# Kernel tuning notes

Measured on AMD Instinct MI355X. Metric: run time of the kernel, lower is better.

Reference implementation:

```python
import jax, jax.numpy as jnp
import numpy as np

B, I, O, H = 16384, 32, 64, 64  # batch, inp_dim, out_dim (towers), hidden width


def setup_inputs() -> dict:
    key = jax.random.key(0)
    ks = jax.random.split(key, 5)
    s0 = 1.0 / np.sqrt(I)
    sh = 1.0 / np.sqrt(H)
    return {
        "x": jax.random.normal(ks[0], (B, I), dtype=jnp.float32),
        "W0": jax.random.normal(ks[1], (O, I, H), dtype=jnp.float32) * s0,
        "b0": jnp.zeros((O, H), dtype=jnp.float32),
        "W1": jax.random.normal(ks[2], (O, H, H), dtype=jnp.float32) * sh,
        "b1": jnp.zeros((O, H), dtype=jnp.float32),
        "W2": jax.random.normal(ks[3], (O, H, H), dtype=jnp.float32) * sh,
        "b2": jnp.zeros((O, H), dtype=jnp.float32),
        "W3": jax.random.normal(ks[4], (O, H), dtype=jnp.float32) * sh,
        "b3": jnp.zeros((O,), dtype=jnp.float32),
    }


def reference(x, W0, b0, W1, b1, W2, b2, W3, b3):
    # O independent towers: Dense(H,relu) x3 then Dense(1); concat along axis=1.
    # Expressed as batched einsums over the tower axis 'o' (same math as the loop).
    h = jax.nn.relu(jnp.einsum('bi,oih->boh', x, W0) + b0)   # [B,O,H]
    h = jax.nn.relu(jnp.einsum('boh,ohk->bok', h, W1) + b1)  # [B,O,H]
    h = jax.nn.relu(jnp.einsum('boh,ohk->bok', h, W2) + b2)  # [B,O,H]
    out = jnp.einsum('boh,oh->bo', h, W3) + b3               # [B,O]
    return out
```

## Files before the change

kernel.cpp:

```cpp
#include <hip/hip_runtime.h>


typedef float  f32x4 __attribute__((ext_vector_type(4)));
typedef _Float16 h8  __attribute__((ext_vector_type(8)));
typedef unsigned int uint4v __attribute__((ext_vector_type(4)));

static constexpr int Bsz  = 16384;
static constexpr int Idim = 32;
static constexpr int Odim = 64;
static constexpr int BPT  = 8;
static constexpr int ROWTILES = (Bsz / 64) / BPT;

static constexpr int IMG = 21504;

#define GLD16(gp, lp) __builtin_amdgcn_global_load_lds( \
    (const __attribute__((address_space(1))) void*)(gp), \
    (__attribute__((address_space(3))) void*)(lp), 16, 0, 0)

__device__ __forceinline__ unsigned short f2h(float f) {
    _Float16 h = (_Float16)f;
    return __builtin_bit_cast(unsigned short, h);
}

__device__ __forceinline__ unsigned cvt_relu_pk(float lo, float hi) {
    unsigned v = __builtin_bit_cast(unsigned, __builtin_amdgcn_cvt_pkrtz(lo, hi));
    unsigned r;
    asm("v_pk_max_f16 %0, %1, 0" : "=v"(r) : "v"(v));
    return r;
}

__device__ __forceinline__ unsigned cvt_pk2(float lo, float hi) {
    return __builtin_bit_cast(unsigned, __builtin_amdgcn_cvt_pkrtz(lo, hi));
}

__device__ __forceinline__ int pi_slot(int in) {
    return 32 * (in >> 5) + 8 * ((in >> 2) & 3) + 4 * ((in >> 4) & 1) + (in & 3);
}

__global__ __launch_bounds__(256) void prep_kernel(
    const float* __restrict__ W0, const float* __restrict__ b0,
    const float* __restrict__ W1, const float* __restrict__ b1,
    const float* __restrict__ W2, const float* __restrict__ b2,
    const float* __restrict__ W3, char* __restrict__ ws)
{
    const int o = blockIdx.x >> 2, q = blockIdx.x & 3, tid = threadIdx.x;
    char* img = ws + o * IMG;
    unsigned short* Wt0 = (unsigned short*)img;
    unsigned short* Wt1 = (unsigned short*)(img + 4096);
    unsigned short* Wt2 = (unsigned short*)(img + 12288);
    unsigned short* w3s = (unsigned short*)(img + 20480);
    float*          bsf = (float*)(img + 20608);

    {
        int f = q * 256 + tid;
        f32x4 v1 = *(const f32x4*)&W1[o * 4096 + f * 4];
        f32x4 v2 = *(const f32x4*)&W2[o * 4096 + f * 4];
        int in = (f * 4) >> 6;
        int h0 = (f * 4) & 63;
        int S  = pi_slot(in);
#pragma unroll
        for (int j = 0; j < 4; ++j) {
            int h = h0 + j;
            int cw = S ^ ((((h >> 2) ^ h) & 7) << 3);
            Wt1[h * 64 + cw] = f2h(v1[j]);
            Wt2[h * 64 + cw] = f2h(v2[j]);
        }
    }
    if (q < 2) {
        int f = q * 256 + tid;
        f32x4 v = *(const f32x4*)&W0[o * 2048 + f * 4];
        int i  = (f * 4) >> 6;
        int h0 = (f * 4) & 63;
#pragma unroll
        for (int j = 0; j < 4; ++j) {
            int h = h0 + j;
            Wt0[h * 32 + (i ^ ((((h >> 2) ^ h) & 3) << 3))] = f2h(v[j]);
        }
    }
    if (q == 3 && tid < 64) {
        w3s[pi_slot(tid)] = f2h(W3[o * 64 + tid]);
        bsf[tid]       = b0[o * 64 + tid];
        bsf[64 + tid]  = b1[o * 64 + tid];
        bsf[128 + tid] = b2[o * 64 + tid];
    }
}

__global__ __launch_bounds__(256, 2) void towers_kernel(
    const float* __restrict__ x, const char* __restrict__ ws,
    const float* __restrict__ b3, float* __restrict__ out)
{
    __shared__ __align__(16) char SH[IMG];

    const int tid  = threadIdx.x;
    const int o    = blockIdx.x / BPT;
    const int slot = blockIdx.x % BPT;
    const int l = tid & 63, w = tid >> 6;
    const int c = l & 15,  g = l >> 4;

    const float* xbase = x + (slot * ROWTILES * 64 + w * 16 + c) * Idim + g * 8;
    f32x4 nxa0 = *(const f32x4*)(xbase);
    f32x4 nxb0 = *(const f32x4*)(xbase + 4);
    f32x4 nxa1 = *(const f32x4*)(xbase + 2048);
    f32x4 nxb1 = *(const f32x4*)(xbase + 2052);

    {
        const char* img = ws + o * IMG;
#pragma unroll
        for (int ch = 0; ch < 6; ++ch) {
            int k = ch * 4 + w;
            if (k < 21)
                GLD16(img + k * 1024 + l * 16, SH + k * 1024);
        }
    }
    __syncthreads();

    const unsigned short* Wt0 = (const unsigned short*)SH;
    const unsigned short* Wt1 = (const unsigned short*)(SH + 4096);
    const unsigned short* w3s = (const unsigned short*)(SH + 20480);
    const float*          bsf = (const float*)(SH + 20608);

    h8 wf0[4], wf1f[4][2];
#pragma unroll
    for (int n = 0; n < 4; ++n) {
        int h = n * 16 + c;
        wf0[n] = *(const h8*)&Wt0[h * 32 + ((g * 8) ^ ((((h >> 2) ^ h) & 3) << 3))];
        int key = ((h >> 2) ^ h) & 7;
#pragma unroll
        for (int s = 0; s < 2; ++s)
            wf1f[n][s] = *(const h8*)&Wt1[h * 64 + ((s * 32 + g * 8) ^ (key << 3))];
    }
    h8 w3a[2];
    w3a[0] = *(const h8*)&w3s[g * 8];
    w3a[1] = *(const h8*)&w3s[32 + g * 8];

    int off2[4][2];
#pragma unroll
    for (int n = 0; n < 4; ++n) {
        int h = n * 16 + c;
        int key = ((h >> 2) ^ h) & 7;
#pragma unroll
        for (int s = 0; s < 2; ++s)
            off2[n][s] = 12288 + 2 * (h * 64 + ((s * 32 + g * 8) ^ (key << 3)));
    }

    f32x4 b0f[4], b1f[4], b2f[4];
#pragma unroll
    for (int n = 0; n < 4; ++n) {
        b0f[n] = *(const f32x4*)&bsf[      n * 16 + g * 4];
        b1f[n] = *(const f32x4*)&bsf[ 64 + n * 16 + g * 4];
        b2f[n] = *(const f32x4*)&bsf[128 + n * 16 + g * 4];
    }
    f32x4 c3 = {0.f, 0.f, 0.f, 0.f};
    if (g == 0) c3[0] = b3[o];

    float* obase = out + (slot * ROWTILES * 64 + w * 16 + c) * Odim + o;

    for (int tt = 0; tt < ROWTILES; tt += 2) {
        f32x4 xa0 = nxa0, xb0 = nxb0, xa1 = nxa1, xb1 = nxb1;
        if (tt + 2 < ROWTILES) {
            const float* np = xbase + (tt + 2) * 2048;
            nxa0 = *(const f32x4*)(np);
            nxb0 = *(const f32x4*)(np + 4);
            nxa1 = *(const f32x4*)(np + 2048);
            nxb1 = *(const f32x4*)(np + 2052);
        }

        uint4v xd0, xd1;
        xd0.x = cvt_pk2(xa0[0], xa0[1]); xd0.y = cvt_pk2(xa0[2], xa0[3]);
        xd0.z = cvt_pk2(xb0[0], xb0[1]); xd0.w = cvt_pk2(xb0[2], xb0[3]);
        xd1.x = cvt_pk2(xa1[0], xa1[1]); xd1.y = cvt_pk2(xa1[2], xa1[3]);
        xd1.z = cvt_pk2(xb1[0], xb1[1]); xd1.w = cvt_pk2(xb1[2], xb1[3]);
        h8 a0_0 = __builtin_bit_cast(h8, xd0);
        h8 a0_1 = __builtin_bit_cast(h8, xd1);

        f32x4 acc0[4], acc1[4];
#pragma unroll
        for (int n = 0; n < 4; ++n) {
            acc0[n] = __builtin_amdgcn_mfma_f32_16x16x32_f16(wf0[n], a0_0, b0f[n], 0, 0, 0);
            acc1[n] = __builtin_amdgcn_mfma_f32_16x16x32_f16(wf0[n], a0_1, b0f[n], 0, 0, 0);
        }

        unsigned p0[4][2], p1[4][2];
#pragma unroll
        for (int n = 0; n < 4; ++n) {
            p0[n][0] = cvt_relu_pk(acc0[n][0], acc0[n][1]);
            p0[n][1] = cvt_relu_pk(acc0[n][2], acc0[n][3]);
            p1[n][0] = cvt_relu_pk(acc1[n][0], acc1[n][1]);
            p1[n][1] = cvt_relu_pk(acc1[n][2], acc1[n][3]);
        }
        h8 Blo0 = __builtin_bit_cast(h8, uint4v{p0[0][0], p0[0][1], p0[1][0], p0[1][1]});
        h8 Bhi0 = __builtin_bit_cast(h8, uint4v{p0[2][0], p0[2][1], p0[3][0], p0[3][1]});
        h8 Blo1 = __builtin_bit_cast(h8, uint4v{p1[0][0], p1[0][1], p1[1][0], p1[1][1]});
        h8 Bhi1 = __builtin_bit_cast(h8, uint4v{p1[2][0], p1[2][1], p1[3][0], p1[3][1]});

#pragma unroll
        for (int n = 0; n < 4; ++n) {
            acc0[n] = __builtin_amdgcn_mfma_f32_16x16x32_f16(wf1f[n][0], Blo0, b1f[n], 0, 0, 0);
            acc1[n] = __builtin_amdgcn_mfma_f32_16x16x32_f16(wf1f[n][0], Blo1, b1f[n], 0, 0, 0);
            acc0[n] = __builtin_amdgcn_mfma_f32_16x16x32_f16(wf1f[n][1], Bhi0, acc0[n], 0, 0, 0);
            acc1[n] = __builtin_amdgcn_mfma_f32_16x16x32_f16(wf1f[n][1], Bhi1, acc1[n], 0, 0, 0);
        }
#pragma unroll
        for (int n = 0; n < 4; ++n) {
            p0[n][0] = cvt_relu_pk(acc0[n][0], acc0[n][1]);
            p0[n][1] = cvt_relu_pk(acc0[n][2], acc0[n][3]);
            p1[n][0] = cvt_relu_pk(acc1[n][0], acc1[n][1]);
            p1[n][1] = cvt_relu_pk(acc1[n][2], acc1[n][3]);
        }
        Blo0 = __builtin_bit_cast(h8, uint4v{p0[0][0], p0[0][1], p0[1][0], p0[1][1]});
        Bhi0 = __builtin_bit_cast(h8, uint4v{p0[2][0], p0[2][1], p0[3][0], p0[3][1]});
        Blo1 = __builtin_bit_cast(h8, uint4v{p1[0][0], p1[0][1], p1[1][0], p1[1][1]});
        Bhi1 = __builtin_bit_cast(h8, uint4v{p1[2][0], p1[2][1], p1[3][0], p1[3][1]});

        {
            const char* base = (const char*)SH;
            h8 w2[4];
#pragma unroll
            for (int n = 0; n < 4; ++n) {
                int a = off2[n][0];
                asm("" : "+v"(a));
                w2[n] = *(const h8*)(base + a);
            }
#pragma unroll
            for (int n = 0; n < 4; ++n) {
                acc0[n] = __builtin_amdgcn_mfma_f32_16x16x32_f16(w2[n], Blo0, b2f[n], 0, 0, 0);
                acc1[n] = __builtin_amdgcn_mfma_f32_16x16x32_f16(w2[n], Blo1, b2f[n], 0, 0, 0);
            }
#pragma unroll
            for (int n = 0; n < 4; ++n) {
                int a = off2[n][1];
                asm("" : "+v"(a));
                w2[n] = *(const h8*)(base + a);
            }
#pragma unroll
            for (int n = 0; n < 4; ++n) {
                acc0[n] = __builtin_amdgcn_mfma_f32_16x16x32_f16(w2[n], Bhi0, acc0[n], 0, 0, 0);
                acc1[n] = __builtin_amdgcn_mfma_f32_16x16x32_f16(w2[n], Bhi1, acc1[n], 0, 0, 0);
            }
        }
#pragma unroll
        for (int n = 0; n < 4; ++n) {
            p0[n][0] = cvt_relu_pk(acc0[n][0], acc0[n][1]);
            p0[n][1] = cvt_relu_pk(acc0[n][2], acc0[n][3]);
            p1[n][0] = cvt_relu_pk(acc1[n][0], acc1[n][1]);
            p1[n][1] = cvt_relu_pk(acc1[n][2], acc1[n][3]);
        }
        Blo0 = __builtin_bit_cast(h8, uint4v{p0[0][0], p0[0][1], p0[1][0], p0[1][1]});
        Bhi0 = __builtin_bit_cast(h8, uint4v{p0[2][0], p0[2][1], p0[3][0], p0[3][1]});
        Blo1 = __builtin_bit_cast(h8, uint4v{p1[0][0], p1[0][1], p1[1][0], p1[1][1]});
        Bhi1 = __builtin_bit_cast(h8, uint4v{p1[2][0], p1[2][1], p1[3][0], p1[3][1]});

        f32x4 acc3_0, acc3_1;
        acc3_0 = __builtin_amdgcn_mfma_f32_16x16x32_f16(w3a[0], Blo0, c3,     0, 0, 0);
        acc3_1 = __builtin_amdgcn_mfma_f32_16x16x32_f16(w3a[0], Blo1, c3,     0, 0, 0);
        acc3_0 = __builtin_amdgcn_mfma_f32_16x16x32_f16(w3a[1], Bhi0, acc3_0, 0, 0, 0);
        acc3_1 = __builtin_amdgcn_mfma_f32_16x16x32_f16(w3a[1], Bhi1, acc3_1, 0, 0, 0);

        if (g == 0) {
            obase[(tt)     * 64 * Odim] = acc3_0[0];
            obase[(tt + 1) * 64 * Odim] = acc3_1[0];
        }
    }
}

extern "C" void kernel_launch(void* const* d_in, const int* in_sizes, int n_in,
                              void* d_out, int out_size, void* d_ws, size_t ws_size,
                              hipStream_t stream) {
    const float* x  = (const float*)d_in[0];
    const float* W0 = (const float*)d_in[1];
    const float* b0 = (const float*)d_in[2];
    const float* W1 = (const float*)d_in[3];
    const float* b1 = (const float*)d_in[4];
    const float* W2 = (const float*)d_in[5];
    const float* b2 = (const float*)d_in[6];
    const float* W3 = (const float*)d_in[7];
    const float* b3 = (const float*)d_in[8];
    float* out = (float*)d_out;
    char* ws = (char*)d_ws;

    prep_kernel<<<dim3(Odim * 4), dim3(256), 0, stream>>>(W0, b0, W1, b1, W2, b2, W3, ws);
    towers_kernel<<<dim3(Odim * BPT), dim3(256), 0, stream>>>(x, ws, b3, out);
}
```

Before: 33.00 us.

## Pre-convert x to fp16 in prep kernel and process four row tiles per iteration

```diff
diff --git a/kernel.cpp b/kernel.cpp
--- a/kernel.cpp
+++ b/kernel.cpp
@@ -3,6 +3,7 @@
 
 typedef float  f32x4 __attribute__((ext_vector_type(4)));
 typedef _Float16 h8  __attribute__((ext_vector_type(8)));
+typedef unsigned int uint2v __attribute__((ext_vector_type(2)));
 typedef unsigned int uint4v __attribute__((ext_vector_type(4)));
 
 static constexpr int Bsz  = 16384;
@@ -10,8 +11,10 @@
 static constexpr int Odim = 64;
 static constexpr int BPT  = 8;
 static constexpr int ROWTILES = (Bsz / 64) / BPT;
+static constexpr int TT = 4;
 
 static constexpr int IMG = 21504;
+static constexpr int XH_OFF = 64 * IMG;
 
 #define GLD16(gp, lp) __builtin_amdgcn_global_load_lds( \
     (const __attribute__((address_space(1))) void*)(gp), \
@@ -29,21 +32,28 @@
     return r;
 }
 
-__device__ __forceinline__ unsigned cvt_pk2(float lo, float hi) {
-    return __builtin_bit_cast(unsigned, __builtin_amdgcn_cvt_pkrtz(lo, hi));
-}
-
 __device__ __forceinline__ int pi_slot(int in) {
     return 32 * (in >> 5) + 8 * ((in >> 2) & 3) + 4 * ((in >> 4) & 1) + (in & 3);
 }
 
 __global__ __launch_bounds__(256) void prep_kernel(
+    const float* __restrict__ x,
     const float* __restrict__ W0, const float* __restrict__ b0,
     const float* __restrict__ W1, const float* __restrict__ b1,
     const float* __restrict__ W2, const float* __restrict__ b2,
     const float* __restrict__ W3, char* __restrict__ ws)
 {
-    const int o = blockIdx.x >> 2, q = blockIdx.x & 3, tid = threadIdx.x;
+    const int tid = threadIdx.x;
+    if (blockIdx.x >= 256) {
+        int idx = (blockIdx.x - 256) * 256 + tid;
+        f32x4 v = *(const f32x4*)&x[idx * 4];
+        uint2v d;
+        d.x = (unsigned)f2h(v[0]) | ((unsigned)f2h(v[1]) << 16);
+        d.y = (unsigned)f2h(v[2]) | ((unsigned)f2h(v[3]) << 16);
+        *(uint2v*)(ws + XH_OFF + idx * 8) = d;
+        return;
+    }
+    const int o = blockIdx.x >> 2, q = blockIdx.x & 3;
     char* img = ws + o * IMG;
     unsigned short* Wt0 = (unsigned short*)img;
     unsigned short* Wt1 = (unsigned short*)(img + 4096);
@@ -86,8 +96,8 @@
 }
 
 __global__ __launch_bounds__(256, 2) void towers_kernel(
-    const float* __restrict__ x, const char* __restrict__ ws,
-    const float* __restrict__ b3, float* __restrict__ out)
+    const char* __restrict__ ws, const float* __restrict__ b3,
+    float* __restrict__ out)
 {
     __shared__ __align__(16) char SH[IMG];
 
@@ -97,11 +107,12 @@
     const int l = tid & 63, w = tid >> 6;
     const int c = l & 15,  g = l >> 4;
 
-    const float* xbase = x + (slot * ROWTILES * 64 + w * 16 + c) * Idim + g * 8;
-    f32x4 nxa0 = *(const f32x4*)(xbase);
-    f32x4 nxb0 = *(const f32x4*)(xbase + 4);
-    f32x4 nxa1 = *(const f32x4*)(xbase + 2048);
-    f32x4 nxb1 = *(const f32x4*)(xbase + 2052);
+    const _Float16* xh = (const _Float16*)(ws + XH_OFF);
+    const _Float16* xbase = xh + (slot * ROWTILES * 64 + w * 16 + c) * Idim + g * 8;
+    h8 nxv[TT];
+#pragma unroll
+    for (int k = 0; k < TT; ++k)
+        nxv[k] = *(const h8*)(xbase + k * 2048);
 
     {
         const char* img = ws + o * IMG;
@@ -155,62 +166,60 @@
 
     float* obase = out + (slot * ROWTILES * 64 + w * 16 + c) * Odim + o;
 
-    for (int tt = 0; tt < ROWTILES; tt += 2) {
-        f32x4 xa0 = nxa0, xb0 = nxb0, xa1 = nxa1, xb1 = nxb1;
-        if (tt + 2 < ROWTILES) {
-            const float* np = xbase + (tt + 2) * 2048;
-            nxa0 = *(const f32x4*)(np);
-            nxb0 = *(const f32x4*)(np + 4);
-            nxa1 = *(const f32x4*)(np + 2048);
-            nxb1 = *(const f32x4*)(np + 2052);
-        }
-
-        uint4v xd0, xd1;
-        xd0.x = cvt_pk2(xa0[0], xa0[1]); xd0.y = cvt_pk2(xa0[2], xa0[3]);
-        xd0.z = cvt_pk2(xb0[0], xb0[1]); xd0.w = cvt_pk2(xb0[2], xb0[3]);
-        xd1.x = cvt_pk2(xa1[0], xa1[1]); xd1.y = cvt_pk2(xa1[2], xa1[3]);
-        xd1.z = cvt_pk2(xb1[0], xb1[1]); xd1.w = cvt_pk2(xb1[2], xb1[3]);
-        h8 a0_0 = __builtin_bit_cast(h8, xd0);
-        h8 a0_1 = __builtin_bit_cast(h8, xd1);
-
-        f32x4 acc0[4], acc1[4];
-#pragma unroll
-        for (int n = 0; n < 4; ++n) {
-            acc0[n] = __builtin_amdgcn_mfma_f32_16x16x32_f16(wf0[n], a0_0, b0f[n], 0, 0, 0);
-            acc1[n] = __builtin_amdgcn_mfma_f32_16x16x32_f16(wf0[n], a0_1, b0f[n], 0, 0, 0);
-        }
-
-        unsigned p0[4][2], p1[4][2];
-#pragma unroll
-        for (int n = 0; n < 4; ++n) {
-            p0[n][0] = cvt_relu_pk(acc0[n][0], acc0[n][1]);
-            p0[n][1] = cvt_relu_pk(acc0[n][2], acc0[n][3]);
-            p1[n][0] = cvt_relu_pk(acc1[n][0], acc1[n][1]);
-            p1[n][1] = cvt_relu_pk(acc1[n][2], acc1[n][3]);
-        }
-        h8 Blo0 = __builtin_bit_cast(h8, uint4v{p0[0][0], p0[0][1], p0[1][0], p0[1][1]});
-        h8 Bhi0 = __builtin_bit_cast(h8, uint4v{p0[2][0], p0[2][1], p0[3][0], p0[3][1]});
-        h8 Blo1 = __builtin_bit_cast(h8, uint4v{p1[0][0], p1[0][1], p1[1][0], p1[1][1]});
-        h8 Bhi1 = __builtin_bit_cast(h8, uint4v{p1[2][0], p1[2][1], p1[3][0], p1[3][1]});
-
-#pragma unroll
-        for (int n = 0; n < 4; ++n) {
-            acc0[n] = __builtin_amdgcn_mfma_f32_16x16x32_f16(wf1f[n][0], Blo0, b1f[n], 0, 0, 0);
-            acc1[n] = __builtin_amdgcn_mfma_f32_16x16x32_f16(wf1f[n][0], Blo1, b1f[n], 0, 0, 0);
-            acc0[n] = __builtin_amdgcn_mfma_f32_16x16x32_f16(wf1f[n][1], Bhi0, acc0[n], 0, 0, 0);
-            acc1[n] = __builtin_amdgcn_mfma_f32_16x16x32_f16(wf1f[n][1], Bhi1, acc1[n], 0, 0, 0);
-        }
-#pragma unroll
-        for (int n = 0; n < 4; ++n) {
-            p0[n][0] = cvt_relu_pk(acc0[n][0], acc0[n][1]);
-            p0[n][1] = cvt_relu_pk(acc0[n][2], acc0[n][3]);
-            p1[n][0] = cvt_relu_pk(acc1[n][0], acc1[n][1]);
-            p1[n][1] = cvt_relu_pk(acc1[n][2], acc1[n][3]);
-        }
-        Blo0 = __builtin_bit_cast(h8, uint4v{p0[0][0], p0[0][1], p0[1][0], p0[1][1]});
-        Bhi0 = __builtin_bit_cast(h8, uint4v{p0[2][0], p0[2][1], p0[3][0], p0[3][1]});
-        Blo1 = __builtin_bit_cast(h8, uint4v{p1[0][0], p1[0][1], p1[1][0], p1[1][1]});
-        Bhi1 = __builtin_bit_cast(h8, uint4v{p1[2][0], p1[2][1], p1[3][0], p1[3][1]});
+    for (int tt = 0; tt < ROWTILES; tt += TT) {
+        h8 xv[TT];
+#pragma unroll
+        for (int k = 0; k < TT; ++k) xv[k] = nxv[k];
+        if (tt + TT < ROWTILES) {
+#pragma unroll
+            for (int k = 0; k < TT; ++k)
+                nxv[k] = *(const h8*)(xbase + (tt + TT + k) * 2048);
+        }
+
+        f32x4 acc[TT][4];
+#pragma unroll
+        for (int n = 0; n < 4; ++n)
+#pragma unroll
+            for (int k = 0; k < TT; ++k)
+                acc[k][n] = __builtin_amdgcn_mfma_f32_16x16x32_f16(wf0[n], xv[k], b0f[n], 0, 0, 0);
+
+        h8 blo[TT], bhi[TT];
+#pragma unroll
+        for (int k = 0; k < TT; ++k) {
+            uint4v lo, hi;
+            lo.x = cvt_relu_pk(acc[k][0][0], acc[k][0][1]);
+            lo.y = cvt_relu_pk(acc[k][0][2], acc[k][0][3]);
+            lo.z = cvt_relu_pk(acc[k][1][0], acc[k][1][1]);
+            lo.w = cvt_relu_pk(acc[k][1][2], acc[k][1][3]);
+            hi.x = cvt_relu_pk(acc[k][2][0], acc[k][2][1]);
+            hi.y = cvt_relu_pk(acc[k][2][2], acc[k][2][3]);
+            hi.z = cvt_relu_pk(acc[k][3][0], acc[k][3][1]);
+            hi.w = cvt_relu_pk(acc[k][3][2], acc[k][3][3]);
+            blo[k] = __builtin_bit_cast(h8, lo);
+            bhi[k] = __builtin_bit_cast(h8, hi);
+        }
+
+#pragma unroll
+        for (int n = 0; n < 4; ++n)
+#pragma unroll
+            for (int k = 0; k < TT; ++k) {
+                acc[k][n] = __builtin_amdgcn_mfma_f32_16x16x32_f16(wf1f[n][0], blo[k], b1f[n], 0, 0, 0);
+                acc[k][n] = __builtin_amdgcn_mfma_f32_16x16x32_f16(wf1f[n][1], bhi[k], acc[k][n], 0, 0, 0);
+            }
+#pragma unroll
+        for (int k = 0; k < TT; ++k) {
+            uint4v lo, hi;
+            lo.x = cvt_relu_pk(acc[k][0][0], acc[k][0][1]);
+            lo.y = cvt_relu_pk(acc[k][0][2], acc[k][0][3]);
+            lo.z = cvt_relu_pk(acc[k][1][0], acc[k][1][1]);
+            lo.w = cvt_relu_pk(acc[k][1][2], acc[k][1][3]);
+            hi.x = cvt_relu_pk(acc[k][2][0], acc[k][2][1]);
+            hi.y = cvt_relu_pk(acc[k][2][2], acc[k][2][3]);
+            hi.z = cvt_relu_pk(acc[k][3][0], acc[k][3][1]);
+            hi.w = cvt_relu_pk(acc[k][3][2], acc[k][3][3]);
+            blo[k] = __builtin_bit_cast(h8, lo);
+            bhi[k] = __builtin_bit_cast(h8, hi);
+        }
 
         {
             const char* base = (const char*)SH;
@@ -222,10 +231,10 @@
                 w2[n] = *(const h8*)(base + a);
             }
 #pragma unroll
-            for (int n = 0; n < 4; ++n) {
-                acc0[n] = __builtin_amdgcn_mfma_f32_16x16x32_f16(w2[n], Blo0, b2f[n], 0, 0, 0);
-                acc1[n] = __builtin_amdgcn_mfma_f32_16x16x32_f16(w2[n], Blo1, b2f[n], 0, 0, 0);
-            }
+            for (int n = 0; n < 4; ++n)
+#pragma unroll
+                for (int k = 0; k < TT; ++k)
+                    acc[k][n] = __builtin_amdgcn_mfma_f32_16x16x32_f16(w2[n], blo[k], b2f[n], 0, 0, 0);
 #pragma unroll
             for (int n = 0; n < 4; ++n) {
                 int a = off2[n][1];
@@ -233,32 +242,33 @@
                 w2[n] = *(const h8*)(base + a);
             }
 #pragma unroll
-            for (int n = 0; n < 4; ++n) {
-                acc0[n] = __builtin_amdgcn_mfma_f32_16x16x32_f16(w2[n], Bhi0, acc0[n], 0, 0, 0);
-                acc1[n] = __builtin_amdgcn_mfma_f32_16x16x32_f16(w2[n], Bhi1, acc1[n], 0, 0, 0);
-            }
-        }
-#pragma unroll
-        for (int n = 0; n < 4; ++n) {
-            p0[n][0] = cvt_relu_pk(acc0[n][0], acc0[n][1]);
-            p0[n][1] = cvt_relu_pk(acc0[n][2], acc0[n][3]);
-            p1[n][0] = cvt_relu_pk(acc1[n][0], acc1[n][1]);
-            p1[n][1] = cvt_relu_pk(acc1[n][2], acc1[n][3]);
-        }
-        Blo0 = __builtin_bit_cast(h8, uint4v{p0[0][0], p0[0][1], p0[1][0], p0[1][1]});
-        Bhi0 = __builtin_bit_cast(h8, uint4v{p0[2][0], p0[2][1], p0[3][0], p0[3][1]});
-        Blo1 = __builtin_bit_cast(h8, uint4v{p1[0][0], p1[0][1], p1[1][0], p1[1][1]});
-        Bhi1 = __builtin_bit_cast(h8, uint4v{p1[2][0], p1[2][1], p1[3][0], p1[3][1]});
-
-        f32x4 acc3_0, acc3_1;
-        acc3_0 = __builtin_amdgcn_mfma_f32_16x16x32_f16(w3a[0], Blo0, c3,     0, 0, 0);
-        acc3_1 = __builtin_amdgcn_mfma_f32_16x16x32_f16(w3a[0], Blo1, c3,     0, 0, 0);
-        acc3_0 = __builtin_amdgcn_mfma_f32_16x16x32_f16(w3a[1], Bhi0, acc3_0, 0, 0, 0);
-        acc3_1 = __builtin_amdgcn_mfma_f32_16x16x32_f16(w3a[1], Bhi1, acc3_1, 0, 0, 0);
-
-        if (g == 0) {
-            obase[(tt)     * 64 * Odim] = acc3_0[0];
-            obase[(tt + 1) * 64 * Odim] = acc3_1[0];
+            for (int n = 0; n < 4; ++n)
+#pragma unroll
+                for (int k = 0; k < TT; ++k)
+                    acc[k][n] = __builtin_amdgcn_mfma_f32_16x16x32_f16(w2[n], bhi[k], acc[k][n], 0, 0, 0);
+        }
+#pragma unroll
+        for (int k = 0; k < TT; ++k) {
+            uint4v lo, hi;
+            lo.x = cvt_relu_pk(acc[k][0][0], acc[k][0][1]);
+            lo.y = cvt_relu_pk(acc[k][0][2], acc[k][0][3]);
+            lo.z = cvt_relu_pk(acc[k][1][0], acc[k][1][1]);
+            lo.w = cvt_relu_pk(acc[k][1][2], acc[k][1][3]);
+            hi.x = cvt_relu_pk(acc[k][2][0], acc[k][2][1]);
+            hi.y = cvt_relu_pk(acc[k][2][2], acc[k][2][3]);
+            hi.z = cvt_relu_pk(acc[k][3][0], acc[k][3][1]);
+            hi.w = cvt_relu_pk(acc[k][3][2], acc[k][3][3]);
+            blo[k] = __builtin_bit_cast(h8, lo);
+            bhi[k] = __builtin_bit_cast(h8, hi);
+        }
+
+#pragma unroll
+        for (int k = 0; k < TT; ++k) {
+            f32x4 a3;
+            a3 = __builtin_amdgcn_mfma_f32_16x16x32_f16(w3a[0], blo[k], c3, 0, 0, 0);
+            a3 = __builtin_amdgcn_mfma_f32_16x16x32_f16(w3a[1], bhi[k], a3, 0, 0, 0);
+            if (g == 0)
+                obase[(tt + k) * 64 * Odim] = a3[0];
         }
     }
 }
@@ -278,6 +288,6 @@
     float* out = (float*)d_out;
     char* ws = (char*)d_ws;
 
-    prep_kernel<<<dim3(Odim * 4), dim3(256), 0, stream>>>(W0, b0, W1, b1, W2, b2, W3, ws);
-    towers_kernel<<<dim3(Odim * BPT), dim3(256), 0, stream>>>(x, ws, b3, out);
-}
+    prep_kernel<<<dim3(256 + 512), dim3(256), 0, stream>>>(x, W0, b0, W1, b1, W2, b2, W3, ws);
+    towers_kernel<<<dim3(Odim * BPT), dim3(256), 0, stream>>>(ws, b3, out);
+}
```

New measurement: 30.89 us. -6.4%, faster.
